# Kernel tuning notes

Hardware: AMD Instinct MI355X
Metric: run time of the kernel (lower is better)

The kernel has to match this reference:

```python
import jax, jax.numpy as jnp
import numpy as np
from jax.scipy.special import logsumexp

EPS = 1e-4  # self.epsilon in the original module


def _pairwise_sqdist(a, b):
    # a: [B,n,d], b: [B,m,d] -> [B,n,m]; same math as get_distance (sum_d a^2+b^2-2ab)
    return (jnp.sum(a * a, axis=-1)[:, :, None]
            + jnp.sum(b * b, axis=-1)[:, None, :]
            - 2.0 * jnp.einsum('bnd,bmd->bnm', a, b))


def setup_inputs() -> dict:
    key = jax.random.key(0)
    kx, ky, ka, kb = jax.random.split(key, 4)
    b, t, n, m, d = 4, 16, 2048, 2048, 64
    return {
        'x': jax.random.normal(kx, (b, t, n, d), dtype=jnp.float32),
        'y': jax.random.normal(ky, (b, t, m, d), dtype=jnp.float32),
        'loga': jax.random.normal(ka, (b, t, n), dtype=jnp.float32),
        'logb': jax.random.normal(kb, (b, t, m), dtype=jnp.float32),
    }


def reference(x, y, loga, logb):
    b, t, n, d = x.shape
    m = y.shape[2]
    # time-major for scan
    xt = jnp.moveaxis(x, 1, 0)      # [t,b,n,d]
    yt = jnp.moveaxis(y, 1, 0)      # [t,b,m,d]
    lat = jnp.moveaxis(loga, 1, 0)  # [t,b,n]
    lbt = jnp.moveaxis(logb, 1, 0)  # [t,b,m]

    def step(carry, inp):
        f_prev, g_prev = carry
        x_new, y_new, x_prev, y_prev, la_prev, lb_prev, la_new = inp
        D = _pairwise_sqdist(x_new, y_prev)  # [b,n,m]
        f_new = -EPS * logsumexp((-D + g_prev[:, None, :]) / EPS + lb_prev[:, None, :], axis=2)
        D2 = _pairwise_sqdist(y_new, x_prev)  # [b,m,n]
        g_new = -EPS * logsumexp((-D2 + f_prev[:, None, :]) / EPS + la_prev[:, None, :], axis=2)
        # Original forward passes loga[:, i] for BOTH new_loga and new_logb (faithful).
        # loss is a global sum (scalar) that torch broadcasts into losses[:, i].
        loss = jnp.sum(jnp.exp(la_new) * f_new) + jnp.sum(jnp.exp(la_new) * g_new)
        return (f_new, g_new), (loss, f_new, g_new)

    f0 = jnp.zeros((b, n), x.dtype)
    g0 = jnp.zeros((b, m), x.dtype)
    xs = (xt[1:], yt[1:], xt[:-1], yt[:-1], lat[:-1], lbt[:-1], lat[1:])
    _, (loss_seq, f_seq, g_seq) = jax.lax.scan(step, (f0, g0), xs)

    losses = jnp.concatenate(
        [jnp.zeros((b, 1), x.dtype), jnp.broadcast_to(loss_seq[None, :], (b, t - 1))], axis=1)
    f = jnp.concatenate([f0[:, None, :], jnp.moveaxis(f_seq, 0, 1)], axis=1)  # [b,t,n]
    g = jnp.concatenate([g0[:, None, :], jnp.moveaxis(g_seq, 0, 1)], axis=1)  # [b,t,m]
    return losses, f, g
```

## Files before the change

### kernel.cpp

```cpp
#include <hip/hip_runtime.h>

#define Bq 4
#define Tt 16
#define Nn 2048
#define Dd 64
#define EPSc 1e-4f

typedef __attribute__((ext_vector_type(8))) short bf16x8;
typedef __attribute__((ext_vector_type(4))) float floatx4;

__device__ __forceinline__ unsigned rne_bf16(float f) {
    unsigned u = __float_as_uint(f);
    return (u + 0x7FFFu + ((u >> 16) & 1u)) >> 16;
}

__device__ __forceinline__ void load_lds16(const void* gptr, void* lptr) {
    __builtin_amdgcn_global_load_lds(
        (const __attribute__((address_space(1))) unsigned int*)gptr,
        (__attribute__((address_space(3))) unsigned int*)lptr,
        16, 0, 0);
}

__device__ __forceinline__ void stage16k(const short* __restrict__ gh,
                                         const short* __restrict__ gl,
                                         short* lh, short* ll, int w, int l)
{
#pragma unroll
    for (int it = 0; it < 2; ++it) {
        const int id = w * 2 + it;
        load_lds16((const char*)gh + id * 1024 + l * 16, (char*)lh + id * 1024);
        load_lds16((const char*)gl + id * 1024 + l * 16, (char*)ll + id * 1024);
    }
}

__global__ void convert_kernel(const float* __restrict__ x, const float* __restrict__ y,
                               short* __restrict__ xh, short* __restrict__ xl,
                               short* __restrict__ yh, short* __restrict__ yl,
                               float* __restrict__ sqx, float* __restrict__ sqy,
                               float* __restrict__ pf0, float* __restrict__ pg0,
                               float* __restrict__ out_f, float* __restrict__ out_g,
                               float* __restrict__ loss_ws)
{
    const int tid = threadIdx.x;
    const int l = tid & 63;
    const int row = blockIdx.x * 32 + (tid >> 6) * 8 + (l >> 3);
    const int q = l & 7;
    const size_t dst = (size_t)row * 64 + (size_t)((q ^ (row & 7)) << 3);

    const float4* px = reinterpret_cast<const float4*>(x + (size_t)row * 64 + q * 8);
    float4 u0 = px[0], u1 = px[1];
    float fx[8] = {u0.x, u0.y, u0.z, u0.w, u1.x, u1.y, u1.z, u1.w};
    bf16x8 hv, lv;
    float ssx = 0.f;
#pragma unroll
    for (int e = 0; e < 8; ++e) {
        unsigned hb = rne_bf16(fx[e]);
        float hf = __uint_as_float(hb << 16);
        unsigned lb = rne_bf16(fx[e] - hf);
        hv[e] = (short)hb;
        lv[e] = (short)lb;
        ssx = fmaf(fx[e], fx[e], ssx);
    }
    *reinterpret_cast<bf16x8*>(&xh[dst]) = hv;
    *reinterpret_cast<bf16x8*>(&xl[dst]) = lv;
    ssx += __shfl_xor(ssx, 1, 64);
    ssx += __shfl_xor(ssx, 2, 64);
    ssx += __shfl_xor(ssx, 4, 64);

    const float4* py = reinterpret_cast<const float4*>(y + (size_t)row * 64 + q * 8);
    float4 v0 = py[0], v1 = py[1];
    float fy[8] = {v0.x, v0.y, v0.z, v0.w, v1.x, v1.y, v1.z, v1.w};
    float ssy = 0.f;
#pragma unroll
    for (int e = 0; e < 8; ++e) {
        unsigned hb = rne_bf16(fy[e]);
        float hf = __uint_as_float(hb << 16);
        unsigned lb = rne_bf16(fy[e] - hf);
        hv[e] = (short)hb;
        lv[e] = (short)lb;
        ssy = fmaf(fy[e], fy[e], ssy);
    }
    *reinterpret_cast<bf16x8*>(&yh[dst]) = hv;
    *reinterpret_cast<bf16x8*>(&yl[dst]) = lv;
    ssy += __shfl_xor(ssy, 1, 64);
    ssy += __shfl_xor(ssy, 2, 64);
    ssy += __shfl_xor(ssy, 4, 64);

    if (q == 0) {
        sqx[row] = ssx;
        sqy[row] = ssy;
        const int t = (row >> 11) & 15, b = row >> 15, n = row & (Nn - 1);
        if (t == 0) {
            out_f[(size_t)b * Tt * Nn + n] = 0.f;
            out_g[(size_t)b * Tt * Nn + n] = 0.f;
#pragma unroll
            for (int h = 0; h < 2; ++h) {
                pf0[((size_t)b * 2 + h) * Nn + n] = -ssx;
                pg0[((size_t)b * 2 + h) * Nn + n] = -ssy;
            }
        }
    }
    if (blockIdx.x == 0 && tid < Tt) loss_ws[tid] = 0.f;
}

__launch_bounds__(512, 2)
__global__ void minmat_kernel(const short* __restrict__ xh, const short* __restrict__ xl,
                              const short* __restrict__ yh, const short* __restrict__ yl,
                              const float* __restrict__ loga, const float* __restrict__ logb,
                              const float* __restrict__ sqx, const float* __restrict__ sqy,
                              const float* __restrict__ pf_in, const float* __restrict__ pg_in,
                              float* __restrict__ pf_out, float* __restrict__ pg_out,
                              float* __restrict__ out_f, float* __restrict__ out_g,
                              float* __restrict__ loss_ws, int s)
{
    __shared__ __align__(16) short Ah[8192], Al[8192];
    __shared__ __align__(16) short Bh[2][8192], Bl[2][8192];
    __shared__ float carr[1024];
    __shared__ float redm[512];

    const int tid = threadIdx.x;
    const int w = tid >> 6, l = tid & 63;
    const int flat = blockIdx.x;
    const int z = flat & 7;
    const int b = z >> 1;
    const int which = (z & 1) ^ (s & 1);
    const int rr0 = flat >> 3;
    const int i0 = (rr0 & 15) * 128;
    const int jh = rr0 >> 4;
    const int jbase = jh * 1024;

    const size_t curm = ((size_t)b * Tt + s) * Nn;
    const size_t prvm = curm - Nn;

    const short* Ahs = (which ? yh : xh) + (curm + i0) * Dd;
    const short* Als = (which ? yl : xl) + (curm + i0) * Dd;
    const short* Bhs = (which ? xh : yh) + (prvm + jbase) * Dd;
    const short* Bls = (which ? xl : yl) + (prvm + jbase) * Dd;
    const float* pin = which ? pf_in : pg_in;
    float* pout      = which ? pg_out : pf_out;
    const float* clog = which ? loga : logb;

    stage16k(Ahs, Als, Ah, Al, w, l);
    stage16k(Bhs, Bls, Bh[0], Bl[0], w, l);

    if (s >= 2 && tid < 32) {
        const int fr = flat * 32 + tid;
        const int fb = fr >> 11, fi = fr & (Nn - 1);
        const size_t fidx = ((size_t)fb * Tt + (s - 1)) * Nn + fi;
        const float mf = fminf(pf_in[((size_t)fb * 2) * Nn + fi],
                               pf_in[((size_t)fb * 2 + 1) * Nn + fi]);
        const float mg = fminf(pg_in[((size_t)fb * 2) * Nn + fi],
                               pg_in[((size_t)fb * 2 + 1) * Nn + fi]);
        const float fn = sqx[fidx] + mf, gn = sqy[fidx] + mg;
        out_f[fidx] = fn;
        out_g[fidx] = gn;
        float contrib = expf(loga[fidx]) * (fn + gn);
#pragma unroll
        for (int off = 16; off > 0; off >>= 1)
            contrib += __shfl_down(contrib, off, 64);
        if (tid == 0) atomicAdd(&loss_ws[s - 1], contrib);
    }

#pragma unroll
    for (int e = 0; e < 2; ++e) {
        const int jj = tid * 2 + e;
        const float p0 = pin[((size_t)b * 2) * Nn + jbase + jj];
        const float p1 = pin[((size_t)b * 2 + 1) * Nn + jbase + jj];
        carr[jj] = -fminf(p0, p1) - EPSc * clog[prvm + jbase + jj];
    }
    __syncthreads();

    const int wr = w >> 2, wc = w & 3;
    const int m0 = wr * 64, n0 = wc * 32;
    const int r15 = l & 15, g = l >> 4;
    const int swq = r15 & 7;

    bf16x8 ahreg[2][4], alreg[2][4];
#pragma unroll
    for (int kc = 0; kc < 2; ++kc) {
        const int koff = (((kc << 2) | g) ^ swq) << 3;
#pragma unroll
        for (int m = 0; m < 4; ++m) {
            const int ra = (m0 + m * 16 + r15) * 64 + koff;
            ahreg[kc][m] = *reinterpret_cast<const bf16x8*>(&Ah[ra]);
            alreg[kc][m] = *reinterpret_cast<const bf16x8*>(&Al[ra]);
        }
    }

    float mm[4][4];
#pragma unroll
    for (int m = 0; m < 4; ++m)
#pragma unroll
        for (int r2 = 0; r2 < 4; ++r2) mm[m][r2] = 1e30f;

    for (int t = 0; t < 8; ++t) {
        const int p = t & 1;
        if (t < 7)
            stage16k(Bhs + (size_t)(t + 1) * 8192, Bls + (size_t)(t + 1) * 8192,
                     Bh[p ^ 1], Bl[p ^ 1], w, l);

        bf16x8 bhr[2][2], blr[2][2];
#pragma unroll
        for (int kc = 0; kc < 2; ++kc) {
            const int koff = (((kc << 2) | g) ^ swq) << 3;
#pragma unroll
            for (int nn = 0; nn < 2; ++nn) {
                const int rb = (n0 + nn * 16 + r15) * 64 + koff;
                bhr[kc][nn] = *reinterpret_cast<const bf16x8*>(&Bh[p][rb]);
                blr[kc][nn] = *reinterpret_cast<const bf16x8*>(&Bl[p][rb]);
            }
        }

        floatx4 acc[4][2];
#pragma unroll
        for (int m = 0; m < 4; ++m)
#pragma unroll
            for (int nn = 0; nn < 2; ++nn)
                acc[m][nn] = floatx4{0.f, 0.f, 0.f, 0.f};

#pragma unroll
        for (int kc = 0; kc < 2; ++kc)
#pragma unroll
            for (int m = 0; m < 4; ++m)
#pragma unroll
                for (int nn = 0; nn < 2; ++nn) {
                    acc[m][nn] = __builtin_amdgcn_mfma_f32_16x16x32_bf16(ahreg[kc][m], bhr[kc][nn], acc[m][nn], 0, 0, 0);
                    acc[m][nn] = __builtin_amdgcn_mfma_f32_16x16x32_bf16(ahreg[kc][m], blr[kc][nn], acc[m][nn], 0, 0, 0);
                    acc[m][nn] = __builtin_amdgcn_mfma_f32_16x16x32_bf16(alreg[kc][m], bhr[kc][nn], acc[m][nn], 0, 0, 0);
                }

        const float cv0 = carr[t * 128 + n0 + r15];
        const float cv1 = carr[t * 128 + n0 + 16 + r15];
#pragma unroll
        for (int m = 0; m < 4; ++m)
#pragma unroll
            for (int r2 = 0; r2 < 4; ++r2) {
                const float v = fminf(fmaf(-2.f, acc[m][0][r2], cv0),
                                      fmaf(-2.f, acc[m][1][r2], cv1));
                mm[m][r2] = fminf(mm[m][r2], v);
            }
        __syncthreads();
    }

#pragma unroll
    for (int off = 1; off < 16; off <<= 1)
#pragma unroll
        for (int m = 0; m < 4; ++m)
#pragma unroll
            for (int r2 = 0; r2 < 4; ++r2)
                mm[m][r2] = fminf(mm[m][r2], __shfl_xor(mm[m][r2], off, 64));

    if (r15 == 0) {
#pragma unroll
        for (int m = 0; m < 4; ++m)
#pragma unroll
            for (int r2 = 0; r2 < 4; ++r2)
                redm[wc * 128 + m0 + m * 16 + g * 4 + r2] = mm[m][r2];
    }
    __syncthreads();
    if (tid < 128) {
        const float v = fminf(fminf(redm[tid], redm[128 + tid]),
                              fminf(redm[256 + tid], redm[384 + tid]));
        pout[((size_t)b * 2 + jh) * Nn + i0 + tid] = v;
    }
}

__global__ void finish_kernel(int u,
                              const float* __restrict__ pf, const float* __restrict__ pg,
                              const float* __restrict__ sqx, const float* __restrict__ sqy,
                              const float* __restrict__ loga,
                              float* __restrict__ out_f, float* __restrict__ out_g,
                              float* __restrict__ loss_ws)
{
    __shared__ float red8[8];
    const int tid = threadIdx.x;
    const int r = blockIdx.x * 512 + tid;
    const int b = r >> 11, i = r & (Nn - 1);
    const size_t idx = ((size_t)b * Tt + u) * Nn + i;
    const float mf = fminf(pf[((size_t)b * 2) * Nn + i], pf[((size_t)b * 2 + 1) * Nn + i]);
    const float mg = fminf(pg[((size_t)b * 2) * Nn + i], pg[((size_t)b * 2 + 1) * Nn + i]);
    const float fn = sqx[idx] + mf, gn = sqy[idx] + mg;
    out_f[idx] = fn;
    out_g[idx] = gn;
    float contrib = expf(loga[idx]) * (fn + gn);
#pragma unroll
    for (int off = 32; off > 0; off >>= 1)
        contrib += __shfl_down(contrib, off, 64);
    if ((tid & 63) == 0) red8[tid >> 6] = contrib;
    __syncthreads();
    if (tid == 0) {
        float ssum = 0.f;
#pragma unroll
        for (int k = 0; k < 8; ++k) ssum += red8[k];
        atomicAdd(&loss_ws[u], ssum);
    }
}

__global__ void final_kernel(float* __restrict__ out_losses, const float* __restrict__ loss_ws)
{
    const int tid = threadIdx.x;
    const int t = tid & 15;
    out_losses[tid] = (t == 0) ? 0.f : loss_ws[t];
}

extern "C" void kernel_launch(void* const* d_in, const int* in_sizes, int n_in,
                              void* d_out, int out_size, void* d_ws, size_t ws_size,
                              hipStream_t stream)
{
    const float* x    = (const float*)d_in[0];
    const float* y    = (const float*)d_in[1];
    const float* loga = (const float*)d_in[2];
    const float* logb = (const float*)d_in[3];

    float* out        = (float*)d_out;
    float* out_losses = out;
    float* out_f      = out + Bq * Tt;
    float* out_g      = out_f + (size_t)Bq * Tt * Nn;

    const size_t NROW = (size_t)Bq * Tt * Nn;
    short* xh = (short*)d_ws;
    short* xl = xh + NROW * Dd;
    short* yh = xl + NROW * Dd;
    short* yl = yh + NROW * Dd;
    float* sqx = (float*)(yl + NROW * Dd);
    float* sqy = sqx + NROW;
    const size_t PM = (size_t)Bq * 2 * Nn;
    float* pf0 = sqy + NROW;
    float* pg0 = pf0 + PM;
    float* pf1 = pg0 + PM;
    float* pg1 = pf1 + PM;
    float* loss_ws = pg1 + PM;

    convert_kernel<<<4096, 256, 0, stream>>>(x, y, xh, xl, yh, yl,
                                             sqx, sqy, pf0, pg0,
                                             out_f, out_g, loss_ws);

    for (int s = 1; s < Tt; ++s) {
        const float* pf_in = (s & 1) ? pf0 : pf1;
        const float* pg_in = (s & 1) ? pg0 : pg1;
        float* pf_out = (s & 1) ? pf1 : pf0;
        float* pg_out = (s & 1) ? pg1 : pg0;
        minmat_kernel<<<256, 512, 0, stream>>>(xh, xl, yh, yl, loga, logb,
                                               sqx, sqy, pf_in, pg_in,
                                               pf_out, pg_out,
                                               out_f, out_g, loss_ws, s);
    }
    finish_kernel<<<16, 512, 0, stream>>>(15, pf1, pg1, sqx, sqy, loga,
                                          out_f, out_g, loss_ws);
    final_kernel<<<1, 64, 0, stream>>>(out_losses, loss_ws);
}
```

Baseline: 365.7 us.

## Replace split-bf16 MFMA distance matmul with per-row scaled split-int8 MFMA

Quantizes x and y rows into a two-level int8 representation (a high byte plus a residual byte at 1/254 the scale) with a per-row scale, replacing the bf16 hi/lo split. The min-plus distance kernel now uses i32 16x16x64 int8 MFMAs, which covers the full 64-wide K in one instruction. LDS staging and global traffic are halved, and the B-tile pipeline now uses explicit vmcnt waits and raw barriers. The risk is reduced precision: an effective ~15-bit mantissa relative to the row max, where eps=1e-4 makes the min sensitive to error.

```diff
diff --git a/kernel.cpp b/kernel.cpp
--- a/kernel.cpp
+++ b/kernel.cpp
@@ -6,12 +6,10 @@
 #define Dd 64
 #define EPSc 1e-4f
 
-typedef __attribute__((ext_vector_type(8))) short bf16x8;
-typedef __attribute__((ext_vector_type(4))) float floatx4;
-
-__device__ __forceinline__ unsigned rne_bf16(float f) {
-    unsigned u = __float_as_uint(f);
-    return (u + 0x7FFFu + ((u >> 16) & 1u)) >> 16;
+typedef __attribute__((ext_vector_type(4))) int intx4;
+
+__device__ __forceinline__ int pack4i(int a, int b, int c, int d) {
+    return (a & 255) | ((b & 255) << 8) | ((c & 255) << 16) | ((d & 255) << 24);
 }
 
 __device__ __forceinline__ void load_lds16(const void* gptr, void* lptr) {
@@ -21,21 +19,14 @@
         16, 0, 0);
 }
 
-__device__ __forceinline__ void stage16k(const short* __restrict__ gh,
-                                         const short* __restrict__ gl,
-                                         short* lh, short* ll, int w, int l)
-{
-#pragma unroll
-    for (int it = 0; it < 2; ++it) {
-        const int id = w * 2 + it;
-        load_lds16((const char*)gh + id * 1024 + l * 16, (char*)lh + id * 1024);
-        load_lds16((const char*)gl + id * 1024 + l * 16, (char*)ll + id * 1024);
-    }
+__device__ __forceinline__ void stage8k(const char* __restrict__ g, char* lds, int w, int l) {
+    load_lds16(g + w * 1024 + l * 16, lds + w * 1024);
 }
 
 __global__ void convert_kernel(const float* __restrict__ x, const float* __restrict__ y,
-                               short* __restrict__ xh, short* __restrict__ xl,
-                               short* __restrict__ yh, short* __restrict__ yl,
+                               char* __restrict__ qxh, char* __restrict__ qxl,
+                               char* __restrict__ qyh, char* __restrict__ qyl,
+                               float* __restrict__ sxs, float* __restrict__ sys,
                                float* __restrict__ sqx, float* __restrict__ sqy,
                                float* __restrict__ pf0, float* __restrict__ pg0,
                                float* __restrict__ out_f, float* __restrict__ out_g,
@@ -45,48 +36,80 @@
     const int l = tid & 63;
     const int row = blockIdx.x * 32 + (tid >> 6) * 8 + (l >> 3);
     const int q = l & 7;
-    const size_t dst = (size_t)row * 64 + (size_t)((q ^ (row & 7)) << 3);
+    const int g = q >> 1;
+    const int sw = (row >> 1) & 3;
+    const size_t dstb = (size_t)row * 64 + ((g ^ sw) << 4) + (q & 1) * 8;
 
     const float4* px = reinterpret_cast<const float4*>(x + (size_t)row * 64 + q * 8);
     float4 u0 = px[0], u1 = px[1];
     float fx[8] = {u0.x, u0.y, u0.z, u0.w, u1.x, u1.y, u1.z, u1.w};
-    bf16x8 hv, lv;
-    float ssx = 0.f;
+    float ssx = 0.f, amx = 0.f;
 #pragma unroll
     for (int e = 0; e < 8; ++e) {
-        unsigned hb = rne_bf16(fx[e]);
-        float hf = __uint_as_float(hb << 16);
-        unsigned lb = rne_bf16(fx[e] - hf);
-        hv[e] = (short)hb;
-        lv[e] = (short)lb;
         ssx = fmaf(fx[e], fx[e], ssx);
-    }
-    *reinterpret_cast<bf16x8*>(&xh[dst]) = hv;
-    *reinterpret_cast<bf16x8*>(&xl[dst]) = lv;
-    ssx += __shfl_xor(ssx, 1, 64);
-    ssx += __shfl_xor(ssx, 2, 64);
-    ssx += __shfl_xor(ssx, 4, 64);
+        amx = fmaxf(amx, fabsf(fx[e]));
+    }
+#pragma unroll
+    for (int d = 1; d < 8; d <<= 1) {
+        ssx += __shfl_xor(ssx, d, 64);
+        amx = fmaxf(amx, __shfl_xor(amx, d, 64));
+    }
+    amx = fmaxf(amx, 1e-8f);
+    const float s1x = amx * (1.f / 127.f);
+    const float i1x = 127.f / amx;
+    const float i2x = i1x * 254.f;
+    int ih[8], il[8];
+#pragma unroll
+    for (int e = 0; e < 8; ++e) {
+        float hq = rintf(fx[e] * i1x);
+        hq = fminf(fmaxf(hq, -127.f), 127.f);
+        ih[e] = (int)hq;
+        const float r = fmaf(-s1x, hq, fx[e]);
+        float lq = rintf(r * i2x);
+        lq = fminf(fmaxf(lq, -127.f), 127.f);
+        il[e] = (int)lq;
+    }
+    *reinterpret_cast<int2*>(qxh + dstb) = make_int2(pack4i(ih[0], ih[1], ih[2], ih[3]),
+                                                    pack4i(ih[4], ih[5], ih[6], ih[7]));
+    *reinterpret_cast<int2*>(qxl + dstb) = make_int2(pack4i(il[0], il[1], il[2], il[3]),
+                                                    pack4i(il[4], il[5], il[6], il[7]));
 
     const float4* py = reinterpret_cast<const float4*>(y + (size_t)row * 64 + q * 8);
     float4 v0 = py[0], v1 = py[1];
     float fy[8] = {v0.x, v0.y, v0.z, v0.w, v1.x, v1.y, v1.z, v1.w};
-    float ssy = 0.f;
+    float ssy = 0.f, amy = 0.f;
 #pragma unroll
     for (int e = 0; e < 8; ++e) {
-        unsigned hb = rne_bf16(fy[e]);
-        float hf = __uint_as_float(hb << 16);
-        unsigned lb = rne_bf16(fy[e] - hf);
-        hv[e] = (short)hb;
-        lv[e] = (short)lb;
         ssy = fmaf(fy[e], fy[e], ssy);
-    }
-    *reinterpret_cast<bf16x8*>(&yh[dst]) = hv;
-    *reinterpret_cast<bf16x8*>(&yl[dst]) = lv;
-    ssy += __shfl_xor(ssy, 1, 64);
-    ssy += __shfl_xor(ssy, 2, 64);
-    ssy += __shfl_xor(ssy, 4, 64);
+        amy = fmaxf(amy, fabsf(fy[e]));
+    }
+#pragma unroll
+    for (int d = 1; d < 8; d <<= 1) {
+        ssy += __shfl_xor(ssy, d, 64);
+        amy = fmaxf(amy, __shfl_xor(amy, d, 64));
+    }
+    amy = fmaxf(amy, 1e-8f);
+    const float s1y = amy * (1.f / 127.f);
+    const float i1y = 127.f / amy;
+    const float i2y = i1y * 254.f;
+#pragma unroll
+    for (int e = 0; e < 8; ++e) {
+        float hq = rintf(fy[e] * i1y);
+        hq = fminf(fmaxf(hq, -127.f), 127.f);
+        ih[e] = (int)hq;
+        const float r = fmaf(-s1y, hq, fy[e]);
+        float lq = rintf(r * i2y);
+        lq = fminf(fmaxf(lq, -127.f), 127.f);
+        il[e] = (int)lq;
+    }
+    *reinterpret_cast<int2*>(qyh + dstb) = make_int2(pack4i(ih[0], ih[1], ih[2], ih[3]),
+                                                    pack4i(ih[4], ih[5], ih[6], ih[7]));
+    *reinterpret_cast<int2*>(qyl + dstb) = make_int2(pack4i(il[0], il[1], il[2], il[3]),
+                                                    pack4i(il[4], il[5], il[6], il[7]));
 
     if (q == 0) {
+        sxs[row] = s1x;
+        sys[row] = s1y;
         sqx[row] = ssx;
         sqy[row] = ssy;
         const int t = (row >> 11) & 15, b = row >> 15, n = row & (Nn - 1);
@@ -104,8 +127,9 @@
 }
 
 __launch_bounds__(512, 2)
-__global__ void minmat_kernel(const short* __restrict__ xh, const short* __restrict__ xl,
-                              const short* __restrict__ yh, const short* __restrict__ yl,
+__global__ void minmat_kernel(const char* __restrict__ qxh, const char* __restrict__ qxl,
+                              const char* __restrict__ qyh, const char* __restrict__ qyl,
+                              const float* __restrict__ sxs, const float* __restrict__ sys,
                               const float* __restrict__ loga, const float* __restrict__ logb,
                               const float* __restrict__ sqx, const float* __restrict__ sqy,
                               const float* __restrict__ pf_in, const float* __restrict__ pg_in,
@@ -113,9 +137,11 @@
                               float* __restrict__ out_f, float* __restrict__ out_g,
                               float* __restrict__ loss_ws, int s)
 {
-    __shared__ __align__(16) short Ah[8192], Al[8192];
-    __shared__ __align__(16) short Bh[2][8192], Bl[2][8192];
-    __shared__ float carr[1024];
+    __shared__ __align__(16) char Ah[8192], Al[8192];
+    __shared__ __align__(16) char Bh[2][8192], Bl[2][8192];
+    __shared__ __align__(16) float carr[1024];
+    __shared__ __align__(16) float tarr[1024];
+    __shared__ __align__(16) float sarr[128];
     __shared__ float redm[512];
 
     const int tid = threadIdx.x;
@@ -132,16 +158,137 @@
     const size_t curm = ((size_t)b * Tt + s) * Nn;
     const size_t prvm = curm - Nn;
 
-    const short* Ahs = (which ? yh : xh) + (curm + i0) * Dd;
-    const short* Als = (which ? yl : xl) + (curm + i0) * Dd;
-    const short* Bhs = (which ? xh : yh) + (prvm + jbase) * Dd;
-    const short* Bls = (which ? xl : yl) + (prvm + jbase) * Dd;
-    const float* pin = which ? pf_in : pg_in;
-    float* pout      = which ? pg_out : pf_out;
-    const float* clog = which ? loga : logb;
-
-    stage16k(Ahs, Als, Ah, Al, w, l);
-    stage16k(Bhs, Bls, Bh[0], Bl[0], w, l);
+    const char* Ahs = (which ? qyh : qxh) + (curm + i0) * 64;
+    const char* Als = (which ? qyl : qxl) + (curm + i0) * 64;
+    const char* Bhs = (which ? qxh : qyh) + (prvm + jbase) * 64;
+    const char* Bls = (which ? qxl : qyl) + (prvm + jbase) * 64;
+    const float* ascale = (which ? sys : sxs) + curm + i0;
+    const float* bscale = (which ? sxs : sys) + prvm + jbase;
+    const float* pin  = which ? pf_in : pg_in;
+    float* pout       = which ? pg_out : pf_out;
+    const float* clog = (which ? loga : logb) + prvm + jbase;
+
+    stage8k(Ahs, Ah, w, l);
+    stage8k(Als, Al, w, l);
+    stage8k(Bhs, Bh[0], w, l);
+    stage8k(Bls, Bl[0], w, l);
+
+#pragma unroll
+    for (int e = 0; e < 2; ++e) {
+        const int jj = tid * 2 + e;
+        const float p0 = pin[((size_t)b * 2) * Nn + jbase + jj];
+        const float p1 = pin[((size_t)b * 2 + 1) * Nn + jbase + jj];
+        carr[jj] = -fminf(p0, p1) - EPSc * clog[jj];
+        tarr[jj] = bscale[jj];
+    }
+    if (tid < 128) sarr[tid] = ascale[tid];
+    __syncthreads();
+
+    const int wr = w >> 2, wc = w & 3;
+    const int m0 = wr * 64, n0 = wc * 32;
+    const int r15 = l & 15, g = l >> 4;
+    const int csel = ((g ^ ((r15 >> 1) & 3)) << 4);
+
+    intx4 ahr[4], alr[4];
+#pragma unroll
+    for (int m = 0; m < 4; ++m) {
+        const int ra = (m0 + m * 16 + r15) * 64 + csel;
+        ahr[m] = *reinterpret_cast<const intx4*>(&Ah[ra]);
+        alr[m] = *reinterpret_cast<const intx4*>(&Al[ra]);
+    }
+    float4 srow4[4];
+#pragma unroll
+    for (int m = 0; m < 4; ++m)
+        srow4[m] = *reinterpret_cast<const float4*>(&sarr[m0 + m * 16 + g * 4]);
+
+    float mm[4][4];
+#pragma unroll
+    for (int m = 0; m < 4; ++m)
+#pragma unroll
+        for (int r2 = 0; r2 < 4; ++r2) mm[m][r2] = 1e30f;
+
+    const float inv254 = 1.f / 254.f;
+
+    for (int t = 0; t < 8; ++t) {
+        const int p = t & 1;
+        if (t < 7) {
+            stage8k(Bhs + (size_t)(t + 1) * 8192, Bh[p ^ 1], w, l);
+            stage8k(Bls + (size_t)(t + 1) * 8192, Bl[p ^ 1], w, l);
+            asm volatile("s_waitcnt vmcnt(2)" ::: "memory");
+        } else {
+            asm volatile("s_waitcnt vmcnt(0)" ::: "memory");
+        }
+        __builtin_amdgcn_s_barrier();
+        asm volatile("" ::: "memory");
+
+        intx4 bhr[2], blr[2];
+#pragma unroll
+        for (int nn = 0; nn < 2; ++nn) {
+            const int rb = (n0 + nn * 16 + r15) * 64 + csel;
+            bhr[nn] = *reinterpret_cast<const intx4*>(&Bh[p][rb]);
+            blr[nn] = *reinterpret_cast<const intx4*>(&Bl[p][rb]);
+        }
+
+        intx4 acc1[4][2], acc2[4][2];
+#pragma unroll
+        for (int m = 0; m < 4; ++m)
+#pragma unroll
+            for (int nn = 0; nn < 2; ++nn) {
+                acc1[m][nn] = intx4{0, 0, 0, 0};
+                acc2[m][nn] = intx4{0, 0, 0, 0};
+            }
+#pragma unroll
+        for (int m = 0; m < 4; ++m)
+#pragma unroll
+            for (int nn = 0; nn < 2; ++nn) {
+                acc1[m][nn] = __builtin_amdgcn_mfma_i32_16x16x64_i8(ahr[m], bhr[nn], acc1[m][nn], 0, 0, 0);
+                acc2[m][nn] = __builtin_amdgcn_mfma_i32_16x16x64_i8(ahr[m], blr[nn], acc2[m][nn], 0, 0, 0);
+                acc2[m][nn] = __builtin_amdgcn_mfma_i32_16x16x64_i8(alr[m], bhr[nn], acc2[m][nn], 0, 0, 0);
+            }
+
+        const int jt = t * 128 + n0;
+        const float cv0 = carr[jt + r15];
+        const float cv1 = carr[jt + 16 + r15];
+        const float tm0 = -2.f * tarr[jt + r15];
+        const float tm1 = -2.f * tarr[jt + 16 + r15];
+#pragma unroll
+        for (int m = 0; m < 4; ++m) {
+            const float* sr = reinterpret_cast<const float*>(&srow4[m]);
+#pragma unroll
+            for (int r2 = 0; r2 < 4; ++r2) {
+                const float p0f = fmaf(inv254, (float)acc2[m][0][r2], (float)acc1[m][0][r2]);
+                const float p1f = fmaf(inv254, (float)acc2[m][1][r2], (float)acc1[m][1][r2]);
+                const float v0 = fmaf(sr[r2] * tm0, p0f, cv0);
+                const float v1 = fmaf(sr[r2] * tm1, p1f, cv1);
+                mm[m][r2] = fminf(mm[m][r2], fminf(v0, v1));
+            }
+        }
+        asm volatile("" ::: "memory");
+        __builtin_amdgcn_s_barrier();
+        asm volatile("" ::: "memory");
+    }
+
+#pragma unroll
+    for (int off = 1; off < 16; off <<= 1)
+#pragma unroll
+        for (int m = 0; m < 4; ++m)
+#pragma unroll
+            for (int r2 = 0; r2 < 4; ++r2)
+                mm[m][r2] = fminf(mm[m][r2], __shfl_xor(mm[m][r2], off, 64));
+
+    if (r15 == 0) {
+#pragma unroll
+        for (int m = 0; m < 4; ++m)
+#pragma unroll
+            for (int r2 = 0; r2 < 4; ++r2)
+                redm[wc * 128 + m0 + m * 16 + g * 4 + r2] = mm[m][r2];
+    }
+    __syncthreads();
+    if (tid < 128) {
+        const float v = fminf(fminf(redm[tid], redm[128 + tid]),
+                              fminf(redm[256 + tid], redm[384 + tid]));
+        pout[((size_t)b * 2 + jh) * Nn + i0 + tid] = v;
+    }
 
     if (s >= 2 && tid < 32) {
         const int fr = flat * 32 + tid;
@@ -160,109 +307,6 @@
             contrib += __shfl_down(contrib, off, 64);
         if (tid == 0) atomicAdd(&loss_ws[s - 1], contrib);
     }
-
-#pragma unroll
-    for (int e = 0; e < 2; ++e) {
-        const int jj = tid * 2 + e;
-        const float p0 = pin[((size_t)b * 2) * Nn + jbase + jj];
-        const float p1 = pin[((size_t)b * 2 + 1) * Nn + jbase + jj];
-        carr[jj] = -fminf(p0, p1) - EPSc * clog[prvm + jbase + jj];
-    }
-    __syncthreads();
-
-    const int wr = w >> 2, wc = w & 3;
-    const int m0 = wr * 64, n0 = wc * 32;
-    const int r15 = l & 15, g = l >> 4;
-    const int swq = r15 & 7;
-
-    bf16x8 ahreg[2][4], alreg[2][4];
-#pragma unroll
-    for (int kc = 0; kc < 2; ++kc) {
-        const int koff = (((kc << 2) | g) ^ swq) << 3;
-#pragma unroll
-        for (int m = 0; m < 4; ++m) {
-            const int ra = (m0 + m * 16 + r15) * 64 + koff;
-            ahreg[kc][m] = *reinterpret_cast<const bf16x8*>(&Ah[ra]);
-            alreg[kc][m] = *reinterpret_cast<const bf16x8*>(&Al[ra]);
-        }
-    }
-
-    float mm[4][4];
-#pragma unroll
-    for (int m = 0; m < 4; ++m)
-#pragma unroll
-        for (int r2 = 0; r2 < 4; ++r2) mm[m][r2] = 1e30f;
-
-    for (int t = 0; t < 8; ++t) {
-        const int p = t & 1;
-        if (t < 7)
-            stage16k(Bhs + (size_t)(t + 1) * 8192, Bls + (size_t)(t + 1) * 8192,
-                     Bh[p ^ 1], Bl[p ^ 1], w, l);
-
-        bf16x8 bhr[2][2], blr[2][2];
-#pragma unroll
-        for (int kc = 0; kc < 2; ++kc) {
-            const int koff = (((kc << 2) | g) ^ swq) << 3;
-#pragma unroll
-            for (int nn = 0; nn < 2; ++nn) {
-                const int rb = (n0 + nn * 16 + r15) * 64 + koff;
-                bhr[kc][nn] = *reinterpret_cast<const bf16x8*>(&Bh[p][rb]);
-                blr[kc][nn] = *reinterpret_cast<const bf16x8*>(&Bl[p][rb]);
-            }
-        }
-
-        floatx4 acc[4][2];
-#pragma unroll
-        for (int m = 0; m < 4; ++m)
-#pragma unroll
-            for (int nn = 0; nn < 2; ++nn)
-                acc[m][nn] = floatx4{0.f, 0.f, 0.f, 0.f};
-
-#pragma unroll
-        for (int kc = 0; kc < 2; ++kc)
-#pragma unroll
-            for (int m = 0; m < 4; ++m)
-#pragma unroll
-                for (int nn = 0; nn < 2; ++nn) {
-                    acc[m][nn] = __builtin_amdgcn_mfma_f32_16x16x32_bf16(ahreg[kc][m], bhr[kc][nn], acc[m][nn], 0, 0, 0);
-                    acc[m][nn] = __builtin_amdgcn_mfma_f32_16x16x32_bf16(ahreg[kc][m], blr[kc][nn], acc[m][nn], 0, 0, 0);
-                    acc[m][nn] = __builtin_amdgcn_mfma_f32_16x16x32_bf16(alreg[kc][m], bhr[kc][nn], acc[m][nn], 0, 0, 0);
-                }
-
-        const float cv0 = carr[t * 128 + n0 + r15];
-        const float cv1 = carr[t * 128 + n0 + 16 + r15];
-#pragma unroll
-        for (int m = 0; m < 4; ++m)
-#pragma unroll
-            for (int r2 = 0; r2 < 4; ++r2) {
-                const float v = fminf(fmaf(-2.f, acc[m][0][r2], cv0),
-                                      fmaf(-2.f, acc[m][1][r2], cv1));
-                mm[m][r2] = fminf(mm[m][r2], v);
-            }
-        __syncthreads();
-    }
-
-#pragma unroll
-    for (int off = 1; off < 16; off <<= 1)
-#pragma unroll
-        for (int m = 0; m < 4; ++m)
-#pragma unroll
-            for (int r2 = 0; r2 < 4; ++r2)
-                mm[m][r2] = fminf(mm[m][r2], __shfl_xor(mm[m][r2], off, 64));
-
-    if (r15 == 0) {
-#pragma unroll
-        for (int m = 0; m < 4; ++m)
-#pragma unroll
-            for (int r2 = 0; r2 < 4; ++r2)
-                redm[wc * 128 + m0 + m * 16 + g * 4 + r2] = mm[m][r2];
-    }
-    __syncthreads();
-    if (tid < 128) {
-        const float v = fminf(fminf(redm[tid], redm[128 + tid]),
-                              fminf(redm[256 + tid], redm[384 + tid]));
-        pout[((size_t)b * 2 + jh) * Nn + i0 + tid] = v;
-    }
 }
 
 __global__ void finish_kernel(int u,
@@ -318,11 +362,14 @@
     float* out_g      = out_f + (size_t)Bq * Tt * Nn;
 
     const size_t NROW = (size_t)Bq * Tt * Nn;
-    short* xh = (short*)d_ws;
-    short* xl = xh + NROW * Dd;
-    short* yh = xl + NROW * Dd;
-    short* yl = yh + NROW * Dd;
-    float* sqx = (float*)(yl + NROW * Dd);
+    char* base = (char*)d_ws;
+    char* qxh = base;
+    char* qxl = qxh + NROW * 64;
+    char* qyh = qxl + NROW * 64;
+    char* qyl = qyh + NROW * 64;
+    float* sxs = (float*)(qyl + NROW * 64);
+    float* sys = sxs + NROW;
+    float* sqx = sys + NROW;
     float* sqy = sqx + NROW;
     const size_t PM = (size_t)Bq * 2 * Nn;
     float* pf0 = sqy + NROW;
@@ -331,8 +378,8 @@
     float* pg1 = pf1 + PM;
     float* loss_ws = pg1 + PM;
 
-    convert_kernel<<<4096, 256, 0, stream>>>(x, y, xh, xl, yh, yl,
-                                             sqx, sqy, pf0, pg0,
+    convert_kernel<<<4096, 256, 0, stream>>>(x, y, qxh, qxl, qyh, qyl,
+                                             sxs, sys, sqx, sqy, pf0, pg0,
                                              out_f, out_g, loss_ws);
 
     for (int s = 1; s < Tt; ++s) {
@@ -340,9 +387,9 @@
         const float* pg_in = (s & 1) ? pg0 : pg1;
         float* pf_out = (s & 1) ? pf1 : pf0;
         float* pg_out = (s & 1) ? pg1 : pg0;
-        minmat_kernel<<<256, 512, 0, stream>>>(xh, xl, yh, yl, loga, logb,
-                                               sqx, sqy, pf_in, pg_in,
-                                               pf_out, pg_out,
+        minmat_kernel<<<256, 512, 0, stream>>>(qxh, qxl, qyh, qyl, sxs, sys,
+                                               loga, logb, sqx, sqy,
+                                               pf_in, pg_in, pf_out, pg_out,
                                                out_f, out_g, loss_ws, s);
     }
     finish_kernel<<<16, 512, 0, stream>>>(15, pf1, pg1, sqx, sqy, loga,
```

After: 335.5 us. 1.09x faster.
